# Kernel optimization log

Measured on AMD Instinct MI355X. Metric: run time of the kernel, lower is better.

## Reference

```python
import jax, jax.numpy as jnp
import numpy as np

B, L, D = 4, 16384, 128          # batch, voxels per sample, d_model
DI, DS, DTR, K = 256, 16, 8, 4   # d_inner, d_state, dt_rank, conv kernel
N = B * L
EPS = 1e-5


def setup_inputs() -> dict:
    key = jax.random.key(0)
    ks = jax.random.split(key, 12)
    s = 0.02
    feats = jax.random.normal(ks[0], (N, D), jnp.float32)
    coords_xyz = jax.random.randint(ks[1], (N, 3), 0, 1024, jnp.int32)
    # per-batch Morton permutation + its inverse
    perm = jnp.stack([jax.random.permutation(jax.random.fold_in(ks[2], i), L) for i in range(B)]).astype(jnp.int32)
    inv_perm = jnp.argsort(perm, axis=1).astype(jnp.int32)
    return {
        'feats': feats,
        'pos_w': jax.random.normal(ks[3], (3, D), jnp.float32) * s,
        'pos_b': jnp.zeros((D,), jnp.float32),
        'rms_w': jnp.ones((D,), jnp.float32),
        'in_proj_w': jax.random.normal(ks[4], (D, 2 * DI), jnp.float32) * s,
        'conv_w': jax.random.normal(ks[5], (DI, K), jnp.float32) * s,
        'conv_b': jnp.zeros((DI,), jnp.float32),
        'x_proj_w': jax.random.normal(ks[6], (DI, DTR + 2 * DS), jnp.float32) * s,
        'dt_proj_w': jax.random.normal(ks[7], (DTR, DI), jnp.float32) * s,
        'dt_proj_b': jax.random.normal(ks[8], (DI,), jnp.float32) * 0.1,
        'A_log': jnp.log(jnp.broadcast_to(jnp.arange(1.0, DS + 1.0, dtype=jnp.float32), (DI, DS))),
        'D_param': jnp.ones((DI,), jnp.float32),
        'out_proj_w': jax.random.normal(ks[9], (DI, D), jnp.float32) * s,
        'ln_w': jnp.ones((D,), jnp.float32),
        'ln_b': jnp.zeros((D,), jnp.float32),
        'coords_xyz': coords_xyz,
        'perm': perm,
        'inv_perm': inv_perm,
    }


def _gssm(feats, pos_w, pos_b, rms_w, in_proj_w, conv_w, conv_b, x_proj_w,
          dt_proj_w, dt_proj_b, A_log, D_param, out_proj_w, ln_w, ln_b,
          coords_xyz, perm, inv_perm):
    # positional embedding of voxel coords
    pe = coords_xyz.astype(jnp.float32) @ pos_w + pos_b            # [N, D]
    h = (feats + pe).reshape(B, L, D)
    # gather into Morton order (per-batch fancy index)
    hm = jnp.take_along_axis(h, perm[:, :, None].astype(jnp.int32), axis=1)  # [B, L, D]
    # Mamba block: RMSNorm then mixer (block returns mixer output only)
    x = hm * jax.lax.rsqrt(jnp.mean(hm * hm, axis=-1, keepdims=True) + EPS) * rms_w
    xz = x @ in_proj_w                                             # [B, L, 2*DI]
    xi, z = xz[..., :DI], xz[..., DI:]
    # depthwise causal conv1d, kernel K
    xp = jnp.pad(xi, ((0, 0), (K - 1, 0), (0, 0)))
    xc = conv_b + sum(xp[:, j:j + L, :] * conv_w[:, j] for j in range(K))
    xc = jax.nn.silu(xc)                                           # [B, L, DI]
    dbc = xc @ x_proj_w                                            # [B, L, DTR+2*DS]
    dt, Bm, Cm = dbc[..., :DTR], dbc[..., DTR:DTR + DS], dbc[..., DTR + DS:]
    dt = jax.nn.softplus(dt @ dt_proj_w + dt_proj_b)               # [B, L, DI]
    A = -jnp.exp(A_log)                                            # [DI, DS]

    def step(hst, inp):
        x_t, dt_t, b_t, c_t = inp                                  # [B,DI],[B,DI],[B,DS],[B,DS]
        hst = jnp.exp(dt_t[..., None] * A) * hst + (dt_t * x_t)[..., None] * b_t[:, None, :]
        return hst, jnp.einsum('bds,bs->bd', hst, c_t)

    h0 = jnp.zeros((B, DI, DS), xc.dtype)
    _, ys = jax.lax.scan(step, h0, (xc.transpose(1, 0, 2), dt.transpose(1, 0, 2),
                                    Bm.transpose(1, 0, 2), Cm.transpose(1, 0, 2)))
    y = ys.transpose(1, 0, 2) + xc * D_param                       # [B, L, DI]
    y = y * jax.nn.silu(z)
    out = y @ out_proj_w                                           # [B, L, D]
    # scatter back to original voxel order
    out = jnp.take_along_axis(out, inv_perm[:, :, None].astype(jnp.int32), axis=1).reshape(N, D)
    # post-SSM LayerNorm
    mu = jnp.mean(out, axis=-1, keepdims=True)
    var = jnp.mean((out - mu) ** 2, axis=-1, keepdims=True)
    return (out - mu) * jax.lax.rsqrt(var + EPS) * ln_w + ln_b


def reference(feats, pos_w, pos_b, rms_w, in_proj_w, conv_w, conv_b, x_proj_w,
              dt_proj_w, dt_proj_b, A_log, D_param, out_proj_w, ln_w, ln_b,
              coords_xyz, perm, inv_perm):
    return _gssm(feats, pos_w, pos_b, rms_w, in_proj_w, conv_w, conv_b, x_proj_w,
                 dt_proj_w, dt_proj_b, A_log, D_param, out_proj_w, ln_w, ln_b,
                 coords_xyz, perm, inv_perm)
```

## Files before the change

kernel.cpp:

```cpp
#include <hip/hip_runtime.h>
#include <hip/hip_bf16.h>
#include <math.h>

#define B_   4
#define L_   16384
#define D_   128
#define DI_  256
#define DS_  16
#define DTR_ 8
#define N_   65536
#define NC_  128
#define LC_  128
#define TW_  16
#define TP_  260
#define EPS_ 1e-5f

typedef __hip_bfloat16 bf16;
typedef __attribute__((ext_vector_type(8))) short short8;
typedef __attribute__((ext_vector_type(4))) float f32x4;

__device__ __forceinline__ bool probe_bf16(const void* Dp) {
  return ((const unsigned*)Dp)[0] == 0x3F803F80u;
}
__device__ __forceinline__ float ldin(const void* p, size_t i, bool isb) {
  return isb ? __bfloat162float(((const bf16*)p)[i]) : ((const float*)p)[i];
}
__device__ __forceinline__ float4 ld4(const void* p, size_t i4, bool isb) {
  if (!isb) return ((const float4*)p)[i4];
  const ushort4 v = ((const ushort4*)p)[i4];
  float4 r;
  r.x = __uint_as_float((unsigned)v.x << 16);
  r.y = __uint_as_float((unsigned)v.y << 16);
  r.z = __uint_as_float((unsigned)v.z << 16);
  r.w = __uint_as_float((unsigned)v.w << 16);
  return r;
}
__device__ __forceinline__ void splitbf(float v, ushort& hi, ushort& lo) {
  bf16 h = __float2bfloat16(v);
  float rem = v - __bfloat162float(h);
  bf16 l = __float2bfloat16(rem);
  hi = *(ushort*)&h;
  lo = *(ushort*)&l;
}


__global__ __launch_bounds__(256) void k_xnorm(
    const void* __restrict__ feats, const void* __restrict__ pos_w,
    const void* __restrict__ pos_b, const void* __restrict__ rms_w,
    const int* __restrict__ coords, const int* __restrict__ perm,
    const void* __restrict__ Dprobe,
    ushort* __restrict__ xh, ushort* __restrict__ xl) {
  const bool isb = probe_bf16(Dprobe);
  int wv = threadIdx.x >> 6, lane = threadIdx.x & 63;
  int p = blockIdx.x * 4 + wv;
  int b = p >> 14;
  int srow = b * L_ + perm[p];
  float cx = (float)coords[srow*3+0];
  float cy = (float)coords[srow*3+1];
  float cz = (float)coords[srow*3+2];
  int i0 = lane, i1 = lane + 64;
  float h0 = ldin(feats,(size_t)srow*D_ + i0,isb) + cx*ldin(pos_w,i0,isb) + cy*ldin(pos_w,D_+i0,isb)
           + cz*ldin(pos_w,2*D_+i0,isb) + ldin(pos_b,i0,isb);
  float h1 = ldin(feats,(size_t)srow*D_ + i1,isb) + cx*ldin(pos_w,i1,isb) + cy*ldin(pos_w,D_+i1,isb)
           + cz*ldin(pos_w,2*D_+i1,isb) + ldin(pos_b,i1,isb);
  float ss = h0*h0 + h1*h1;
  #pragma unroll
  for (int off = 32; off; off >>= 1) ss += __shfl_xor(ss, off);
  float r = 1.0f / sqrtf(ss * (1.f/128.f) + EPS_);
  float v0 = h0 * r * ldin(rms_w,i0,isb);
  float v1 = h1 * r * ldin(rms_w,i1,isb);
  ushort a, bq;
  splitbf(v0, a, bq);
  xh[(size_t)p*D_ + i0] = a; xl[(size_t)p*D_ + i0] = bq;
  splitbf(v1, a, bq);
  xh[(size_t)p*D_ + i1] = a; xl[(size_t)p*D_ + i1] = bq;
}

__global__ __launch_bounds__(256) void k_prepw(
    const void* __restrict__ Win, const void* __restrict__ Dprobe,
    ushort* __restrict__ wth, ushort* __restrict__ wtl) {
  const bool isb = probe_bf16(Dprobe);
  int idx = blockIdx.x * 256 + threadIdx.x;
  int k = idx >> 9, n = idx & 511;
  float v = ldin(Win, (size_t)k*512 + n, isb);
  ushort a, b;
  splitbf(v, a, b);
  wth[(size_t)n*128 + k] = a;
  wtl[(size_t)n*128 + k] = b;
}

__global__ __launch_bounds__(256) void k_prepxw(
    const void* __restrict__ xW, const void* __restrict__ Dprobe,
    ushort* __restrict__ wxh, ushort* __restrict__ wxl) {
  const bool isb = probe_bf16(Dprobe);
  int idx = blockIdx.x * 256 + threadIdx.x;
  int q = idx >> 8, c = idx & 255;
  float v = (q < 40) ? ldin(xW, (size_t)c*40 + q, isb) : 0.f;
  ushort a, b;
  splitbf(v, a, b);
  wxh[idx] = a;
  wxl[idx] = b;
}

__global__ __launch_bounds__(256) void k_inproj(
    const ushort* __restrict__ xh, const ushort* __restrict__ xl,
    const ushort* __restrict__ wth, const ushort* __restrict__ wtl,
    float* __restrict__ xiT, float* __restrict__ zB) {
  __shared__ short Ah[64*136];
  __shared__ short Al[64*136];
  __shared__ short Bh[32*136];
  __shared__ short Bl[32*136];
  int tid = threadIdx.x;
  int T0 = blockIdx.x * 64;
  int lane = tid & 63, w = tid >> 6;
  {
    int k0 = (tid & 15) * 8;
    int m0 = tid >> 4;
    #pragma unroll
    for (int mi = 0; mi < 4; ++mi) {
      int m = m0 + 16*mi;
      *(short8*)&Ah[m*136 + k0] = *(const short8*)&xh[(size_t)(T0+m)*128 + k0];
      *(short8*)&Al[m*136 + k0] = *(const short8*)&xl[(size_t)(T0+m)*128 + k0];
    }
  }
  __syncthreads();
  int mloc = lane & 15, quad = lane >> 4;
  short8 afh[4], afl[4];
  #pragma unroll
  for (int ks = 0; ks < 4; ++ks) {
    int ka = ks*32 + quad*8;
    afh[ks] = *(const short8*)&Ah[(w*16 + mloc)*136 + ka];
    afl[ks] = *(const short8*)&Al[(w*16 + mloc)*136 + ka];
  }
  for (int ct = 0; ct < 16; ++ct) {
    int C0 = ct * 32;
    __syncthreads();
    {
      int k0 = (tid & 15) * 8;
      int n0 = tid >> 4;
      #pragma unroll
      for (int ni = 0; ni < 2; ++ni) {
        int n = n0 + 16*ni;
        *(short8*)&Bh[n*136 + k0] = *(const short8*)&wth[(size_t)(C0+n)*128 + k0];
        *(short8*)&Bl[n*136 + k0] = *(const short8*)&wtl[(size_t)(C0+n)*128 + k0];
      }
    }
    __syncthreads();
    #pragma unroll
    for (int nt = 0; nt < 2; ++nt) {
      f32x4 acc = {0.f, 0.f, 0.f, 0.f};
      #pragma unroll
      for (int ks = 0; ks < 4; ++ks) {
        int kb = ks*32 + quad*8;
        short8 bh = *(const short8*)&Bh[(nt*16 + mloc)*136 + kb];
        short8 bl = *(const short8*)&Bl[(nt*16 + mloc)*136 + kb];
        acc = __builtin_amdgcn_mfma_f32_16x16x32_bf16(afh[ks], bh, acc, 0, 0, 0);
        acc = __builtin_amdgcn_mfma_f32_16x16x32_bf16(afl[ks], bh, acc, 0, 0, 0);
        acc = __builtin_amdgcn_mfma_f32_16x16x32_bf16(afh[ks], bl, acc, 0, 0, 0);
      }
      int col = C0 + nt*16 + mloc;
      int trow = T0 + w*16 + quad*4;
      if (col < 256) {
        *(float4*)&xiT[(size_t)col*N_ + trow] = make_float4(acc[0], acc[1], acc[2], acc[3]);
      } else {
        int zc = col - 256;
        #pragma unroll
        for (int r = 0; r < 4; ++r)
          zB[(size_t)(trow + r)*256 + zc] = acc[r];
      }
    }
  }
}

__global__ __launch_bounds__(256) void k_conv_s(
    const float* __restrict__ xiT, const void* __restrict__ conv_w,
    const void* __restrict__ conv_b, const void* __restrict__ Dprobe,
    float* __restrict__ xcT) {
  const bool isb = probe_bf16(Dprobe);
  int idx = blockIdx.x * 256 + threadIdx.x;
  int c = idx >> 16;
  int t = idx & 65535;
  int l = t & (L_-1);
  const float* row = xiT + (size_t)c * N_;
  float acc = ldin(conv_b, c, isb);
  if (l >= 3) acc += row[t-3] * ldin(conv_w, c*4+0, isb);
  if (l >= 2) acc += row[t-2] * ldin(conv_w, c*4+1, isb);
  if (l >= 1) acc += row[t-1] * ldin(conv_w, c*4+2, isb);
  acc += row[t] * ldin(conv_w, c*4+3, isb);
  xcT[(size_t)c*N_ + t] = acc / (1.f + __expf(-acc));
}

__global__ __launch_bounds__(256) void k_xproj(
    const float* __restrict__ xcT,
    const ushort* __restrict__ wxh, const ushort* __restrict__ wxl,
    const void* __restrict__ dtW, const void* __restrict__ dtb,
    const void* __restrict__ Dprobe,
    float* __restrict__ dtT, float* __restrict__ BmB, float* __restrict__ CmB) {
  const bool isb = probe_bf16(Dprobe);
  __shared__ ushort Ah[64*136];
  __shared__ ushort Al[64*136];
  __shared__ float s40[64*52];
  const int tid = threadIdx.x;
  const int lane = tid & 63, w = tid >> 6;
  const int T0 = blockIdx.x * 64;
  const int n15 = lane & 15, quad = lane >> 4;

  short8 afh[8], afl[8];
  #pragma unroll
  for (int kh = 0; kh < 2; ++kh) {
    if (kh) __syncthreads();
    #pragma unroll
    for (int p = 0; p < 4; ++p) {
      int idx = p*256 + tid;
      int cp = idx >> 4;
      int t4 = idx & 15;
      const float* base = &xcT[(size_t)(kh*128 + 2*cp)*N_ + T0 + t4*4];
      float4 v0 = *(const float4*)base;
      float4 v1 = *(const float4*)(base + N_);
      uint* AH = (uint*)Ah;
      uint* AL = (uint*)Al;
      int r0 = t4*4;
      ushort ha, la, hb, lb;
      splitbf(v0.x, ha, la); splitbf(v1.x, hb, lb);
      AH[(r0+0)*68 + cp] = (uint)ha | ((uint)hb << 16);
      AL[(r0+0)*68 + cp] = (uint)la | ((uint)lb << 16);
      splitbf(v0.y, ha, la); splitbf(v1.y, hb, lb);
      AH[(r0+1)*68 + cp] = (uint)ha | ((uint)hb << 16);
      AL[(r0+1)*68 + cp] = (uint)la | ((uint)lb << 16);
      splitbf(v0.z, ha, la); splitbf(v1.z, hb, lb);
      AH[(r0+2)*68 + cp] = (uint)ha | ((uint)hb << 16);
      AL[(r0+2)*68 + cp] = (uint)la | ((uint)lb << 16);
      splitbf(v0.w, ha, la); splitbf(v1.w, hb, lb);
      AH[(r0+3)*68 + cp] = (uint)ha | ((uint)hb << 16);
      AL[(r0+3)*68 + cp] = (uint)la | ((uint)lb << 16);
    }
    __syncthreads();
    {
      int mrow = w*16 + n15;
      #pragma unroll
      for (int ks = 0; ks < 4; ++ks) {
        int ka = ks*32 + quad*8;
        afh[kh*4+ks] = *(const short8*)&Ah[mrow*136 + ka];
        afl[kh*4+ks] = *(const short8*)&Al[mrow*136 + ka];
      }
    }
  }
  #pragma unroll
  for (int nt = 0; nt < 3; ++nt) {
    f32x4 a = {0.f, 0.f, 0.f, 0.f};
    size_t bb = (size_t)(nt*16 + n15)*256 + quad*8;
    #pragma unroll
    for (int ks = 0; ks < 8; ++ks) {
      short8 bh = *(const short8*)&wxh[bb + ks*32];
      short8 bl = *(const short8*)&wxl[bb + ks*32];
      a = __builtin_amdgcn_mfma_f32_16x16x32_bf16(afh[ks], bh, a, 0, 0, 0);
      a = __builtin_amdgcn_mfma_f32_16x16x32_bf16(afl[ks], bh, a, 0, 0, 0);
      a = __builtin_amdgcn_mfma_f32_16x16x32_bf16(afh[ks], bl, a, 0, 0, 0);
    }
    #pragma unroll
    for (int r = 0; r < 4; ++r)
      s40[(w*16 + quad*4 + r)*52 + nt*16 + n15] = a[r];
  }
  __syncthreads();
  {
    int t = tid >> 2, fq = tid & 3;
    float4 bm = *(const float4*)&s40[t*52 + 8  + fq*4];
    float4 cm = *(const float4*)&s40[t*52 + 24 + fq*4];
    *(float4*)&BmB[(size_t)(T0+t)*16 + fq*4] = bm;
    *(float4*)&CmB[(size_t)(T0+t)*16 + fq*4] = cm;
  }
  {
    float4 d0 = *(const float4*)&s40[lane*52 + 0];
    float4 d1 = *(const float4*)&s40[lane*52 + 4];
    float dtv[8] = {d0.x, d0.y, d0.z, d0.w, d1.x, d1.y, d1.z, d1.w};
    #pragma unroll 4
    for (int dd = 0; dd < 64; ++dd) {
      int d = w*64 + dd;
      float pre = ldin(dtb, d, isb);
      #pragma unroll
      for (int r = 0; r < 8; ++r) pre += dtv[r] * ldin(dtW, r*256 + d, isb);
      float sp = (pre > 20.f) ? pre : log1pf(__expf(pre));
      dtT[(size_t)d*N_ + T0 + lane] = sp;
    }
  }
}

__global__ __launch_bounds__(256) void k_scan1(
    const float* __restrict__ dtT, const float* __restrict__ xcT,
    const float* __restrict__ BmB, const void* __restrict__ A_log,
    const void* __restrict__ Dprobe, float* __restrict__ Pb, float* __restrict__ Sb) {
  const bool isb = probe_bf16(Dprobe);
  __shared__ float sdt[TW_*TP_];
  __shared__ float sxc[TW_*TP_];
  __shared__ float sbm[LC_*16];
  int tid = threadIdx.x;
  int blk = blockIdx.x;
  int b = blk >> 7, ch = blk & 127;
  int T0 = b * L_ + ch * LC_;
  int d = tid;
  #pragma unroll
  for (int p = 0; p < 2; ++p) {
    int f = (p*256 + tid) * 4;
    *(float4*)&sbm[f] = *(const float4*)&BmB[(size_t)T0*16 + f];
  }
  float Al[16];
  #pragma unroll
  for (int s = 0; s < 16; ++s) Al[s] = -__expf(ldin(A_log, d*16 + s, isb));
  float h[16];
  #pragma unroll
  for (int s = 0; s < 16; ++s) h[s] = 0.f;
  float sumdt = 0.f;
  for (int it = 0; it < LC_; it += TW_) {
    __syncthreads();
    #pragma unroll
    for (int p = 0; p < 4; ++p) {
      int idx = p*256 + tid;
      int d2 = idx >> 2;
      int i4 = (idx & 3) * 4;
      float4 v = *(const float4*)&dtT[(size_t)d2*N_ + T0 + it + i4];
      float4 w = *(const float4*)&xcT[(size_t)d2*N_ + T0 + it + i4];
      sdt[(i4+0)*TP_ + d2] = v.x; sdt[(i4+1)*TP_ + d2] = v.y;
      sdt[(i4+2)*TP_ + d2] = v.z; sdt[(i4+3)*TP_ + d2] = v.w;
      sxc[(i4+0)*TP_ + d2] = w.x; sxc[(i4+1)*TP_ + d2] = w.y;
      sxc[(i4+2)*TP_ + d2] = w.z; sxc[(i4+3)*TP_ + d2] = w.w;
    }
    __syncthreads();
    #pragma unroll
    for (int i = 0; i < TW_; ++i) {
      float dtv = sdt[i*TP_ + d];
      float xcv = sxc[i*TP_ + d];
      sumdt += dtv;
      float du = dtv * xcv;
      const float* bmr = &sbm[(it+i)*16];
      #pragma unroll
      for (int s = 0; s < 16; ++s)
        h[s] = __expf(dtv * Al[s]) * h[s] + du * bmr[s];
    }
  }
  size_t rec = ((size_t)blk*256 + d) * 16;
  #pragma unroll
  for (int s = 0; s < 16; ++s) {
    Sb[rec + s] = h[s];
    Pb[rec + s] = __expf(Al[s] * sumdt);
  }
}

__global__ __launch_bounds__(256) void k_scan2(
    const float* __restrict__ Pb, const float* __restrict__ Sb, float* __restrict__ Hin) {
  int tid = blockIdx.x * 256 + threadIdx.x;
  int b = tid >> 12, r = tid & 4095;
  float h = 0.f;
  for (int ch = 0; ch < NC_; ++ch) {
    size_t rec = ((size_t)(b*NC_ + ch)) * 4096 + r;
    Hin[rec] = h;
    h = Pb[rec] * h + Sb[rec];
  }
}

__global__ __launch_bounds__(256) void k_scan3(
    const float* __restrict__ dtT, const float* __restrict__ xcT,
    const float* __restrict__ BmB, const float* __restrict__ CmB,
    const void* __restrict__ A_log, const void* __restrict__ Dp,
    const float* __restrict__ Hin, float* __restrict__ zyg) {
  const bool isb = probe_bf16(Dp);
  __shared__ float sdt[TW_*TP_];
  __shared__ float sxc[TW_*TP_];
  __shared__ float sbm[LC_*16];
  __shared__ float scm[LC_*16];
  int tid = threadIdx.x;
  int blk = blockIdx.x;
  int b = blk >> 7, ch = blk & 127;
  int T0 = b * L_ + ch * LC_;
  int d = tid;
  #pragma unroll
  for (int p = 0; p < 2; ++p) {
    int f = (p*256 + tid) * 4;
    *(float4*)&sbm[f] = *(const float4*)&BmB[(size_t)T0*16 + f];
    *(float4*)&scm[f] = *(const float4*)&CmB[(size_t)T0*16 + f];
  }
  float Al[16];
  #pragma unroll
  for (int s = 0; s < 16; ++s) Al[s] = -__expf(ldin(A_log, d*16 + s, isb));
  float h[16];
  size_t rec = ((size_t)blk*256 + d) * 16;
  #pragma unroll
  for (int s = 0; s < 16; ++s) h[s] = Hin[rec + s];
  float Dv = ldin(Dp, d, isb);
  for (int it = 0; it < LC_; it += TW_) {
    __syncthreads();
    #pragma unroll
    for (int p = 0; p < 4; ++p) {
      int idx = p*256 + tid;
      int d2 = idx >> 2;
      int i4 = (idx & 3) * 4;
      float4 v = *(const float4*)&dtT[(size_t)d2*N_ + T0 + it + i4];
      float4 w = *(const float4*)&xcT[(size_t)d2*N_ + T0 + it + i4];
      sdt[(i4+0)*TP_ + d2] = v.x; sdt[(i4+1)*TP_ + d2] = v.y;
      sdt[(i4+2)*TP_ + d2] = v.z; sdt[(i4+3)*TP_ + d2] = v.w;
      sxc[(i4+0)*TP_ + d2] = w.x; sxc[(i4+1)*TP_ + d2] = w.y;
      sxc[(i4+2)*TP_ + d2] = w.z; sxc[(i4+3)*TP_ + d2] = w.w;
    }
    __syncthreads();
    #pragma unroll
    for (int i = 0; i < TW_; ++i) {
      float dtv = sdt[i*TP_ + d];
      float xcv = sxc[i*TP_ + d];
      float du = dtv * xcv;
      const float* bmr = &sbm[(it+i)*16];
      const float* cmr = &scm[(it+i)*16];
      float y = 0.f;
      #pragma unroll
      for (int s = 0; s < 16; ++s) {
        h[s] = __expf(dtv * Al[s]) * h[s] + du * bmr[s];
        y += h[s] * cmr[s];
      }
      float yv = y + xcv * Dv;
      size_t zi = (size_t)(T0 + it + i)*256 + d;
      float zv = zyg[zi];
      float sil = zv / (1.f + __expf(-zv));
      zyg[zi] = yv * sil;
    }
  }
}

__global__ __launch_bounds__(256) void k_outproj(
    const float* __restrict__ yg, const void* __restrict__ W2,
    const void* __restrict__ Dprobe, float* __restrict__ outp) {
  const bool isb = probe_bf16(Dprobe);
  __shared__ float As[64*68];
  __shared__ float Bs[64*128];
  int tid = threadIdx.x;
  int T0 = blockIdx.x * 64;
  int tm = tid & 15, tn = tid >> 4;
  float acc[4][8] = {{0.f}};
  for (int kb = 0; kb < 256; kb += 64) {
    {
      int m = tid & 63, kq = tid >> 6;
      #pragma unroll
      for (int r = 0; r < 4; ++r) {
        int k0 = kq*16 + r*4;
        float4 v = *(const float4*)&yg[(size_t)(T0+m)*256 + kb + k0];
        As[(k0+0)*68+m] = v.x; As[(k0+1)*68+m] = v.y;
        As[(k0+2)*68+m] = v.z; As[(k0+3)*68+m] = v.w;
      }
      int n = (tid & 31)*4, kq2 = tid >> 5;
      #pragma unroll
      for (int p = 0; p < 8; ++p) {
        int k = kq2 + p*8;
        float4 w = ld4(W2, ((size_t)(kb+k)*128 + n) >> 2, isb);
        *(float4*)&Bs[k*128 + n] = w;
      }
    }
    __syncthreads();
    #pragma unroll 4
    for (int k = 0; k < 64; ++k) {
      float4 a  = *(const float4*)&As[k*68 + tm*4];
      float4 b0 = *(const float4*)&Bs[k*128 + tn*8];
      float4 b1 = *(const float4*)&Bs[k*128 + tn*8 + 4];
      float am[4] = {a.x, a.y, a.z, a.w};
      float bn[8] = {b0.x, b0.y, b0.z, b0.w, b1.x, b1.y, b1.z, b1.w};
      #pragma unroll
      for (int mi = 0; mi < 4; ++mi)
        #pragma unroll
        for (int ni = 0; ni < 8; ++ni)
          acc[mi][ni] += am[mi] * bn[ni];
    }
    __syncthreads();
  }
  #pragma unroll
  for (int mi = 0; mi < 4; ++mi) {
    size_t m = (size_t)(T0 + tm*4 + mi);
    *(float4*)&outp[m*128 + tn*8]     = make_float4(acc[mi][0], acc[mi][1], acc[mi][2], acc[mi][3]);
    *(float4*)&outp[m*128 + tn*8 + 4] = make_float4(acc[mi][4], acc[mi][5], acc[mi][6], acc[mi][7]);
  }
}

__global__ __launch_bounds__(256) void k_ln(
    const float* __restrict__ outp, const int* __restrict__ perm,
    const void* __restrict__ ln_w, const void* __restrict__ ln_b,
    const void* __restrict__ Dprobe, void* __restrict__ out) {
  const bool isb = probe_bf16(Dprobe);
  int wv = threadIdx.x >> 6, lane = threadIdx.x & 63;
  int p = blockIdx.x * 4 + wv;
  int b = p >> 14;
  int dest = b * L_ + perm[p];
  float v0 = outp[(size_t)p*128 + lane];
  float v1 = outp[(size_t)p*128 + lane + 64];
  float s1 = v0 + v1, s2 = v0*v0 + v1*v1;
  #pragma unroll
  for (int off = 32; off; off >>= 1) {
    s1 += __shfl_xor(s1, off);
    s2 += __shfl_xor(s2, off);
  }
  float mean = s1 * (1.f/128.f);
  float var  = s2 * (1.f/128.f) - mean*mean;
  float r = 1.0f / sqrtf(var + EPS_);
  float o0 = (v0 - mean)*r*ldin(ln_w,lane,isb)    + ldin(ln_b,lane,isb);
  float o1 = (v1 - mean)*r*ldin(ln_w,lane+64,isb) + ldin(ln_b,lane+64,isb);
  if (isb) {
    ((bf16*)out)[(size_t)dest*128 + lane]      = __float2bfloat16(o0);
    ((bf16*)out)[(size_t)dest*128 + lane + 64] = __float2bfloat16(o1);
  } else {
    ((float*)out)[(size_t)dest*128 + lane]      = o0;
    ((float*)out)[(size_t)dest*128 + lane + 64] = o1;
  }
}

extern "C" void kernel_launch(void* const* d_in, const int* in_sizes, int n_in,
                              void* d_out, int out_size, void* d_ws, size_t ws_size,
                              hipStream_t stream) {
  const void* feats    = d_in[0];
  const void* pos_w    = d_in[1];
  const void* pos_b    = d_in[2];
  const void* rms_w    = d_in[3];
  const void* in_proj  = d_in[4];
  const void* conv_w   = d_in[5];
  const void* conv_b   = d_in[6];
  const void* x_proj   = d_in[7];
  const void* dt_projw = d_in[8];
  const void* dt_projb = d_in[9];
  const void* A_log    = d_in[10];
  const void* D_param  = d_in[11];
  const void* out_proj = d_in[12];
  const void* ln_w     = d_in[13];
  const void* ln_b     = d_in[14];
  const int*  coords   = (const int*)d_in[15];
  const int*  perm     = (const int*)d_in[16];

  float* ws = (float*)d_ws;
  const size_t NN = (size_t)N_;
  ushort* xh  = (ushort*)ws;
  ushort* xl  = (ushort*)(ws + 64*NN);
  ushort* wth = (ushort*)(ws + 640*NN);
  ushort* wtl = (ushort*)(ws + 641*NN);
  ushort* wxh = (ushort*)ws;
  ushort* wxl = ((ushort*)ws) + 48*256;
  float* Pb   = ws;
  float* Sb   = ws + 32*NN;
  float* Hin  = ws + 64*NN;
  float* BmB  = ws + 96*NN;
  float* CmB  = ws + 112*NN;
  float* xiT  = ws + 128*NN;
  float* dtT  = ws + 128*NN;
  float* outp = ws + 128*NN;
  float* zB   = ws + 384*NN;
  float* yg   = zB;
  float* xcT  = ws + 640*NN;

  k_prepw<<<256, 256, 0, stream>>>(in_proj, D_param, wth, wtl);
  k_xnorm<<<N_/4, 256, 0, stream>>>(feats, pos_w, pos_b, rms_w, coords, perm, D_param, xh, xl);
  k_inproj<<<N_/64, 256, 0, stream>>>(xh, xl, wth, wtl, xiT, zB);
  k_prepxw<<<48, 256, 0, stream>>>(x_proj, D_param, wxh, wxl);
  k_conv_s<<<(DI_*N_)/256, 256, 0, stream>>>(xiT, conv_w, conv_b, D_param, xcT);
  k_xproj<<<N_/64, 256, 0, stream>>>(xcT, wxh, wxl, dt_projw, dt_projb, D_param, dtT, BmB, CmB);
  k_scan1<<<B_*NC_, 256, 0, stream>>>(dtT, xcT, BmB, A_log, D_param, Pb, Sb);
  k_scan2<<<64, 256, 0, stream>>>(Pb, Sb, Hin);
  k_scan3<<<B_*NC_, 256, 0, stream>>>(dtT, xcT, BmB, CmB, A_log, D_param, Hin, zB);
  k_outproj<<<N_/64, 256, 0, stream>>>(yg, out_proj, D_param, outp);
  k_ln<<<N_/4, 256, 0, stream>>>(outp, perm, ln_w, ln_b, D_param, d_out);
}
```

Before: 571.5 us.

## Move dt projection onto MFMA and load x_proj operands directly from global

Adds a prep kernel that splits dt_proj weights into bf16 hi/lo halves padded to K=32, so k_xproj can compute the dt projection with split-bf16 MFMA instead of a scalar loop. The scalar loop re-read the weights for every element. The x_proj GEMM is also restructured: xcT is read straight from global memory into register B-operands, and the weights become the A-operand, which removes the LDS staging and transpose. The per-lane strided global loads of xcT may coalesce poorly, and each output is computed once per lane layout, so store patterns to dtT change.

Measured after the change: 557.7 us. -2.4%, faster.

```diff
diff --git a/kernel.cpp b/kernel.cpp
--- a/kernel.cpp
+++ b/kernel.cpp
@@ -100,6 +100,19 @@
   splitbf(v, a, b);
   wxh[idx] = a;
   wxl[idx] = b;
+}
+
+__global__ __launch_bounds__(256) void k_prepdtw(
+    const void* __restrict__ dtW, const void* __restrict__ Dprobe,
+    ushort* __restrict__ dtwh, ushort* __restrict__ dtwl) {
+  const bool isb = probe_bf16(Dprobe);
+  int idx = blockIdx.x * 256 + threadIdx.x;
+  int d = idx >> 5, k = idx & 31;
+  float v = (k < 8) ? ldin(dtW, (size_t)k*256 + d, isb) : 0.f;
+  ushort a, b;
+  splitbf(v, a, b);
+  dtwh[idx] = a;
+  dtwl[idx] = b;
 }
 
 __global__ __launch_bounds__(256) void k_inproj(
@@ -193,73 +206,49 @@
 __global__ __launch_bounds__(256) void k_xproj(
     const float* __restrict__ xcT,
     const ushort* __restrict__ wxh, const ushort* __restrict__ wxl,
-    const void* __restrict__ dtW, const void* __restrict__ dtb,
-    const void* __restrict__ Dprobe,
+    const ushort* __restrict__ dtwh, const ushort* __restrict__ dtwl,
+    const void* __restrict__ dtb, const void* __restrict__ Dprobe,
     float* __restrict__ dtT, float* __restrict__ BmB, float* __restrict__ CmB) {
   const bool isb = probe_bf16(Dprobe);
-  __shared__ ushort Ah[64*136];
-  __shared__ ushort Al[64*136];
   __shared__ float s40[64*52];
+  __shared__ float sdtb[256];
   const int tid = threadIdx.x;
   const int lane = tid & 63, w = tid >> 6;
   const int T0 = blockIdx.x * 64;
   const int n15 = lane & 15, quad = lane >> 4;
-
-  short8 afh[8], afl[8];
-  #pragma unroll
-  for (int kh = 0; kh < 2; ++kh) {
-    if (kh) __syncthreads();
-    #pragma unroll
-    for (int p = 0; p < 4; ++p) {
-      int idx = p*256 + tid;
-      int cp = idx >> 4;
-      int t4 = idx & 15;
-      const float* base = &xcT[(size_t)(kh*128 + 2*cp)*N_ + T0 + t4*4];
-      float4 v0 = *(const float4*)base;
-      float4 v1 = *(const float4*)(base + N_);
-      uint* AH = (uint*)Ah;
-      uint* AL = (uint*)Al;
-      int r0 = t4*4;
-      ushort ha, la, hb, lb;
-      splitbf(v0.x, ha, la); splitbf(v1.x, hb, lb);
-      AH[(r0+0)*68 + cp] = (uint)ha | ((uint)hb << 16);
-      AL[(r0+0)*68 + cp] = (uint)la | ((uint)lb << 16);
-      splitbf(v0.y, ha, la); splitbf(v1.y, hb, lb);
-      AH[(r0+1)*68 + cp] = (uint)ha | ((uint)hb << 16);
-      AL[(r0+1)*68 + cp] = (uint)la | ((uint)lb << 16);
-      splitbf(v0.z, ha, la); splitbf(v1.z, hb, lb);
-      AH[(r0+2)*68 + cp] = (uint)ha | ((uint)hb << 16);
-      AL[(r0+2)*68 + cp] = (uint)la | ((uint)lb << 16);
-      splitbf(v0.w, ha, la); splitbf(v1.w, hb, lb);
-      AH[(r0+3)*68 + cp] = (uint)ha | ((uint)hb << 16);
-      AL[(r0+3)*68 + cp] = (uint)la | ((uint)lb << 16);
-    }
-    __syncthreads();
-    {
-      int mrow = w*16 + n15;
-      #pragma unroll
-      for (int ks = 0; ks < 4; ++ks) {
-        int ka = ks*32 + quad*8;
-        afh[kh*4+ks] = *(const short8*)&Ah[mrow*136 + ka];
-        afl[kh*4+ks] = *(const short8*)&Al[mrow*136 + ka];
-      }
-    }
-  }
-  #pragma unroll
-  for (int nt = 0; nt < 3; ++nt) {
-    f32x4 a = {0.f, 0.f, 0.f, 0.f};
-    size_t bb = (size_t)(nt*16 + n15)*256 + quad*8;
-    #pragma unroll
-    for (int ks = 0; ks < 8; ++ks) {
-      short8 bh = *(const short8*)&wxh[bb + ks*32];
-      short8 bl = *(const short8*)&wxl[bb + ks*32];
-      a = __builtin_amdgcn_mfma_f32_16x16x32_bf16(afh[ks], bh, a, 0, 0, 0);
-      a = __builtin_amdgcn_mfma_f32_16x16x32_bf16(afl[ks], bh, a, 0, 0, 0);
-      a = __builtin_amdgcn_mfma_f32_16x16x32_bf16(afh[ks], bl, a, 0, 0, 0);
-    }
-    #pragma unroll
-    for (int r = 0; r < 4; ++r)
-      s40[(w*16 + quad*4 + r)*52 + nt*16 + n15] = a[r];
+  sdtb[tid] = ldin(dtb, tid, isb);
+
+  f32x4 acc0 = {0.f,0.f,0.f,0.f}, acc1 = {0.f,0.f,0.f,0.f}, acc2 = {0.f,0.f,0.f,0.f};
+  const float* xb = &xcT[(size_t)(quad*8)*N_ + T0 + w*16 + n15];
+  #pragma unroll
+  for (int ks = 0; ks < 8; ++ks) {
+    short8 bh, bl;
+    #pragma unroll
+    for (int j = 0; j < 8; ++j) {
+      ushort h, l;
+      splitbf(xb[(size_t)(ks*32 + j)*N_], h, l);
+      bh[j] = (short)h; bl[j] = (short)l;
+    }
+    #pragma unroll
+    for (int mt = 0; mt < 3; ++mt) {
+      const size_t aoff = (size_t)(mt*16 + n15)*256 + ks*32 + quad*8;
+      short8 ah = *(const short8*)&wxh[aoff];
+      short8 al = *(const short8*)&wxl[aoff];
+      f32x4 a = (mt==0) ? acc0 : (mt==1) ? acc1 : acc2;
+      a = __builtin_amdgcn_mfma_f32_16x16x32_bf16(ah, bh, a, 0, 0, 0);
+      a = __builtin_amdgcn_mfma_f32_16x16x32_bf16(al, bh, a, 0, 0, 0);
+      a = __builtin_amdgcn_mfma_f32_16x16x32_bf16(ah, bl, a, 0, 0, 0);
+      if (mt==0) acc0 = a; else if (mt==1) acc1 = a; else acc2 = a;
+    }
+  }
+  {
+    const int trow = (w*16 + n15)*52;
+    #pragma unroll
+    for (int r = 0; r < 4; ++r) {
+      s40[trow +      quad*4 + r] = acc0[r];
+      s40[trow + 16 + quad*4 + r] = acc1[r];
+      s40[trow + 32 + quad*4 + r] = acc2[r];
+    }
   }
   __syncthreads();
   {
@@ -269,18 +258,28 @@
     *(float4*)&BmB[(size_t)(T0+t)*16 + fq*4] = bm;
     *(float4*)&CmB[(size_t)(T0+t)*16 + fq*4] = cm;
   }
-  {
-    float4 d0 = *(const float4*)&s40[lane*52 + 0];
-    float4 d1 = *(const float4*)&s40[lane*52 + 4];
-    float dtv[8] = {d0.x, d0.y, d0.z, d0.w, d1.x, d1.y, d1.z, d1.w};
-    #pragma unroll 4
-    for (int dd = 0; dd < 64; ++dd) {
-      int d = w*64 + dd;
-      float pre = ldin(dtb, d, isb);
-      #pragma unroll
-      for (int r = 0; r < 8; ++r) pre += dtv[r] * ldin(dtW, r*256 + d, isb);
+  short8 dh, dl;
+  #pragma unroll
+  for (int j = 0; j < 8; ++j) {
+    ushort h, l;
+    splitbf(s40[(w*16 + n15)*52 + quad*8 + j], h, l);
+    dh[j] = (short)h; dl[j] = (short)l;
+  }
+  #pragma unroll
+  for (int mt = 0; mt < 16; ++mt) {
+    f32x4 a = {0.f,0.f,0.f,0.f};
+    const size_t doff = (size_t)(mt*16 + n15)*32 + quad*8;
+    short8 ah = *(const short8*)&dtwh[doff];
+    short8 al = *(const short8*)&dtwl[doff];
+    a = __builtin_amdgcn_mfma_f32_16x16x32_bf16(ah, dh, a, 0, 0, 0);
+    a = __builtin_amdgcn_mfma_f32_16x16x32_bf16(al, dh, a, 0, 0, 0);
+    a = __builtin_amdgcn_mfma_f32_16x16x32_bf16(ah, dl, a, 0, 0, 0);
+    #pragma unroll
+    for (int r = 0; r < 4; ++r) {
+      int d = mt*16 + quad*4 + r;
+      float pre = a[r] + sdtb[d];
       float sp = (pre > 20.f) ? pre : log1pf(__expf(pre));
-      dtT[(size_t)d*N_ + T0 + lane] = sp;
+      dtT[(size_t)d*N_ + T0 + w*16 + n15] = sp;
     }
   }
 }
@@ -533,8 +532,10 @@
   ushort* xl  = (ushort*)(ws + 64*NN);
   ushort* wth = (ushort*)(ws + 640*NN);
   ushort* wtl = (ushort*)(ws + 641*NN);
-  ushort* wxh = (ushort*)ws;
-  ushort* wxl = ((ushort*)ws) + 48*256;
+  ushort* wxh  = (ushort*)ws;
+  ushort* wxl  = ((ushort*)ws) + 12288;
+  ushort* dtwh = ((ushort*)ws) + 24576;
+  ushort* dtwl = ((ushort*)ws) + 32768;
   float* Pb   = ws;
   float* Sb   = ws + 32*NN;
   float* Hin  = ws + 64*NN;
@@ -551,8 +552,9 @@
   k_xnorm<<<N_/4, 256, 0, stream>>>(feats, pos_w, pos_b, rms_w, coords, perm, D_param, xh, xl);
   k_inproj<<<N_/64, 256, 0, stream>>>(xh, xl, wth, wtl, xiT, zB);
   k_prepxw<<<48, 256, 0, stream>>>(x_proj, D_param, wxh, wxl);
+  k_prepdtw<<<32, 256, 0, stream>>>(dt_projw, D_param, dtwh, dtwl);
   k_conv_s<<<(DI_*N_)/256, 256, 0, stream>>>(xiT, conv_w, conv_b, D_param, xcT);
-  k_xproj<<<N_/64, 256, 0, stream>>>(xcT, wxh, wxl, dt_projw, dt_projb, D_param, dtT, BmB, CmB);
+  k_xproj<<<N_/64, 256, 0, stream>>>(xcT, wxh, wxl, dtwh, dtwl, dt_projb, D_param, dtT, BmB, CmB);
   k_scan1<<<B_*NC_, 256, 0, stream>>>(dtT, xcT, BmB, A_log, D_param, Pb, Sb);
   k_scan2<<<64, 256, 0, stream>>>(Pb, Sb, Hin);
   k_scan3<<<B_*NC_, 256, 0, stream>>>(dtT, xcT, BmB, CmB, A_log, D_param, Hin, zB);
```
